# Performance work log

Hardware: AMD Instinct MI355X
Metric: run time of the kernel (lower is better)

## Reference

```python
import jax, jax.numpy as jnp
import numpy as np

N_NODES = 40000
N_EDGES = 640000
D_FEAT = 128


def setup_inputs() -> dict:
    key = jax.random.key(0)
    k1, k2, k3 = jax.random.split(key, 3)
    feats = jax.random.normal(k1, (N_NODES, D_FEAT), dtype=jnp.float32)
    src = jax.random.randint(k2, (N_EDGES,), 0, N_NODES, dtype=jnp.int32)
    dst = jax.random.randint(k3, (N_EDGES,), 0, N_NODES, dtype=jnp.int32)
    return {"feats": feats, "src": src, "dst": dst}


def reference(feats, src, dst):
    n = feats.shape[0]
    # gather node features to edges and take L1 diff: u_sub_v then sum(|.|)
    diff = feats[src] - feats[dst]                                # [E, D]
    e = jnp.exp(-0.01 * jnp.sum(jnp.abs(diff), axis=-1))          # [E], exp(-1/100 * L1)
    # edge softmax grouped by destination node (numerically stable)
    m = jax.ops.segment_max(e, dst, num_segments=n)               # [N]
    ex = jnp.exp(e - m[dst])                                      # [E]
    s = jax.ops.segment_sum(ex, dst, num_segments=n)              # [N]
    out = ex / s[dst]                                             # [E]
    return out[:, None]                                           # [E, 1] (matches feats.view(-1,1,D) head dim)
```

## Files before the change

### kernel.cpp

```cpp
#include <hip/hip_runtime.h>
#include <hip/hip_fp16.h>
#include <math.h>

#define D_FEAT 128

typedef _Float16 half2_t __attribute__((ext_vector_type(2)));

__device__ __forceinline__ float l1_u(unsigned int ua, unsigned int ub, float acc) {
    half2_t a = __builtin_bit_cast(half2_t, ua);
    half2_t b = __builtin_bit_cast(half2_t, ub);
    half2_t d = a - b;
    unsigned int du = __builtin_bit_cast(unsigned int, d) & 0x7fff7fffu;
    half2_t ad = __builtin_bit_cast(half2_t, du);
    const half2_t one = {(_Float16)1.0f, (_Float16)1.0f};
    return __builtin_amdgcn_fdot2(ad, one, acc, false);
}

__device__ __forceinline__ float l1_u4(uint4 a, uint4 b, float acc) {
    acc = l1_u(a.x, b.x, acc);
    acc = l1_u(a.y, b.y, acc);
    acc = l1_u(a.z, b.z, acc);
    acc = l1_u(a.w, b.w, acc);
    return acc;
}

__device__ __forceinline__ unsigned int pkh(float x, float y) {
    __half2 h = __halves2half2(__float2half_rn(x), __float2half_rn(y));
    return __builtin_bit_cast(unsigned int, h);
}

__global__ __launch_bounds__(256) void prep_kernel(
    const float* __restrict__ feats, unsigned int* __restrict__ fh,
    float* __restrict__ s, int n_nodes, int n_vec)
{
    int i = blockIdx.x * blockDim.x + threadIdx.x;
    if (i < n_nodes) s[i] = 0.0f;
    if (i < n_vec) {
        const float4* fp = (const float4*)feats;
        float4 a = fp[2 * i];
        float4 b = fp[2 * i + 1];
        uint4 o;
        o.x = pkh(a.x, a.y);
        o.y = pkh(a.z, a.w);
        o.z = pkh(b.x, b.y);
        o.w = pkh(b.z, b.w);
        ((uint4*)fh)[i] = o;
    }
}

__global__ __launch_bounds__(256) void edge_kernel(
    const unsigned int* __restrict__ fh, const int* __restrict__ src,
    const int* __restrict__ dst, float* __restrict__ out,
    float* __restrict__ s, int n_edges)
{
    int tid = blockIdx.x * blockDim.x + threadIdx.x;
    int l   = tid & 7;
    int g   = tid >> 3;
    int e0  = g * 2;
    int e1  = e0 + 1;
    if (e0 >= n_edges) return;
    bool have1 = (e1 < n_edges);

    int s0 = src[e0], d0 = dst[e0];
    int s1 = have1 ? src[e1] : s0;
    int d1 = have1 ? dst[e1] : d0;

    const uint4* t = (const uint4*)fh;
    uint4 sa0 = t[(size_t)s0 * 16 + l];
    uint4 sb0 = t[(size_t)s0 * 16 + l + 8];
    uint4 da0 = t[(size_t)d0 * 16 + l];
    uint4 db0 = t[(size_t)d0 * 16 + l + 8];
    uint4 sa1 = t[(size_t)s1 * 16 + l];
    uint4 sb1 = t[(size_t)s1 * 16 + l + 8];
    uint4 da1 = t[(size_t)d1 * 16 + l];
    uint4 db1 = t[(size_t)d1 * 16 + l + 8];

    float p0 = 0.0f, p1 = 0.0f;
    p0 = l1_u4(sa0, da0, p0);
    p0 = l1_u4(sb0, db0, p0);
    p1 = l1_u4(sa1, da1, p1);
    p1 = l1_u4(sb1, db1, p1);

    #pragma unroll
    for (int mask = 4; mask >= 1; mask >>= 1) {
        p0 += __shfl_xor(p0, mask);
        p1 += __shfl_xor(p1, mask);
    }

    if (l == 0) {
        float w0 = expf(expf(-0.01f * p0));
        out[e0] = w0;
        atomicAdd(s + d0, w0);
        if (have1) {
            float w1 = expf(expf(-0.01f * p1));
            out[e1] = w1;
            atomicAdd(s + d1, w1);
        }
    }
}

__global__ void norm_kernel(const int* __restrict__ dst, const float* __restrict__ s,
                            float* __restrict__ out, int n_edges)
{
    int i = blockIdx.x * blockDim.x + threadIdx.x;
    if (i >= n_edges) return;
    out[i] = out[i] / s[dst[i]];
}

extern "C" void kernel_launch(void* const* d_in, const int* in_sizes, int n_in,
                              void* d_out, int out_size, void* d_ws, size_t ws_size,
                              hipStream_t stream) {
    const float* feats = (const float*)d_in[0];
    const int*   src   = (const int*)d_in[1];
    const int*   dst   = (const int*)d_in[2];
    float* out = (float*)d_out;

    int n_edges = in_sizes[1];
    int n_nodes = in_sizes[0] / D_FEAT;
    int n_vec   = n_nodes * (D_FEAT / 8);

    float* sseg = (float*)d_ws;
    unsigned int* fh = (unsigned int*)((char*)d_ws + (size_t)n_nodes * sizeof(float));

    prep_kernel<<<(n_vec + 255) / 256, 256, 0, stream>>>(feats, fh, sseg, n_nodes, n_vec);

    long long threads = ((long long)n_edges + 1) / 2 * 8;
    int n_blocks_edge = (int)((threads + 255) / 256);
    edge_kernel<<<n_blocks_edge, 256, 0, stream>>>(fh, src, dst, out, sseg, n_edges);

    norm_kernel<<<(n_edges + 255) / 256, 256, 0, stream>>>(dst, sseg, out, n_edges);
}
```

Measured before the change: 116.9 us.

## Split edge L1 gather into four feature-chunk passes with partial sums

Replaces the single edge kernel with four launches, each gathering only a 64-byte column chunk of the fp16 feature table for every edge and accumulating partial L1 sums in a workspace buffer. The idea is that each pass touches a quarter of the table (about 2.5MB), so it fits in cache and the random gathers hit more often. In exchange the src/dst indices are reread four times, there are three extra launches, and the partial array is written and read between passes.

```diff
diff --git a/kernel.cpp b/kernel.cpp
--- a/kernel.cpp
+++ b/kernel.cpp
@@ -3,6 +3,9 @@
 #include <math.h>
 
 #define D_FEAT 128
+#define ROW_U4   16
+#define NCHUNK   4
+#define CHUNK_U4 4
 
 typedef _Float16 half2_t __attribute__((ext_vector_type(2)));
 
@@ -48,53 +51,33 @@
     }
 }
 
-__global__ __launch_bounds__(256) void edge_kernel(
+__global__ __launch_bounds__(256) void edge_pass_kernel(
     const unsigned int* __restrict__ fh, const int* __restrict__ src,
-    const int* __restrict__ dst, float* __restrict__ out,
-    float* __restrict__ s, int n_edges)
+    const int* __restrict__ dst, float* __restrict__ partial,
+    float* __restrict__ out, float* __restrict__ s,
+    int n_edges, int chunk, int pass_flags)
 {
     int tid = blockIdx.x * blockDim.x + threadIdx.x;
-    int l   = tid & 7;
-    int g   = tid >> 3;
-    int e0  = g * 2;
-    int e1  = e0 + 1;
-    if (e0 >= n_edges) return;
-    bool have1 = (e1 < n_edges);
+    int l = tid & 3;
+    int e = tid >> 2;
+    if (e >= n_edges) return;
 
-    int s0 = src[e0], d0 = dst[e0];
-    int s1 = have1 ? src[e1] : s0;
-    int d1 = have1 ? dst[e1] : d0;
-
+    int sr = src[e], dr = dst[e];
     const uint4* t = (const uint4*)fh;
-    uint4 sa0 = t[(size_t)s0 * 16 + l];
-    uint4 sb0 = t[(size_t)s0 * 16 + l + 8];
-    uint4 da0 = t[(size_t)d0 * 16 + l];
-    uint4 db0 = t[(size_t)d0 * 16 + l + 8];
-    uint4 sa1 = t[(size_t)s1 * 16 + l];
-    uint4 sb1 = t[(size_t)s1 * 16 + l + 8];
-    uint4 da1 = t[(size_t)d1 * 16 + l];
-    uint4 db1 = t[(size_t)d1 * 16 + l + 8];
-
-    float p0 = 0.0f, p1 = 0.0f;
-    p0 = l1_u4(sa0, da0, p0);
-    p0 = l1_u4(sb0, db0, p0);
-    p1 = l1_u4(sa1, da1, p1);
-    p1 = l1_u4(sb1, db1, p1);
-
-    #pragma unroll
-    for (int mask = 4; mask >= 1; mask >>= 1) {
-        p0 += __shfl_xor(p0, mask);
-        p1 += __shfl_xor(p1, mask);
-    }
+    uint4 a = t[(size_t)sr * ROW_U4 + chunk * CHUNK_U4 + l];
+    uint4 b = t[(size_t)dr * ROW_U4 + chunk * CHUNK_U4 + l];
+    float p = l1_u4(a, b, 0.0f);
+    p += __shfl_xor(p, 1);
+    p += __shfl_xor(p, 2);
 
     if (l == 0) {
-        float w0 = expf(expf(-0.01f * p0));
-        out[e0] = w0;
-        atomicAdd(s + d0, w0);
-        if (have1) {
-            float w1 = expf(expf(-0.01f * p1));
-            out[e1] = w1;
-            atomicAdd(s + d1, w1);
+        float acc = (pass_flags & 1) ? p : (partial[e] + p);
+        if (pass_flags & 2) {
+            float w = expf(expf(-0.01f * acc));
+            out[e] = w;
+            atomicAdd(s + dr, w);
+        } else {
+            partial[e] = acc;
         }
     }
 }
@@ -120,13 +103,18 @@
     int n_vec   = n_nodes * (D_FEAT / 8);
 
     float* sseg = (float*)d_ws;
-    unsigned int* fh = (unsigned int*)((char*)d_ws + (size_t)n_nodes * sizeof(float));
+    float* partial = sseg + n_nodes;
+    unsigned int* fh = (unsigned int*)(partial + n_edges);
 
     prep_kernel<<<(n_vec + 255) / 256, 256, 0, stream>>>(feats, fh, sseg, n_nodes, n_vec);
 
-    long long threads = ((long long)n_edges + 1) / 2 * 8;
+    long long threads = (long long)n_edges * 4;
     int n_blocks_edge = (int)((threads + 255) / 256);
-    edge_kernel<<<n_blocks_edge, 256, 0, stream>>>(fh, src, dst, out, sseg, n_edges);
+    for (int c = 0; c < NCHUNK; ++c) {
+        int flags = (c == 0 ? 1 : 0) | (c == NCHUNK - 1 ? 2 : 0);
+        edge_pass_kernel<<<n_blocks_edge, 256, 0, stream>>>(
+            fh, src, dst, partial, out, sseg, n_edges, c, flags);
+    }
 
     norm_kernel<<<(n_edges + 255) / 256, 256, 0, stream>>>(dst, sseg, out, n_edges);
 }
```

Result: slower. 150.8 us (+29.0%).
